# Performance work log

Measured on AMD Instinct MI355X. Metric: run time of the kernel, lower is better.

Reference implementation:

```python
import jax, jax.numpy as jnp
import numpy as np

WS, OWS, HEADS, DIM = 16, 24, 6, 192
PAD = (OWS - WS) // 2
NQ, NKV = WS * WS, OWS * OWS
TABLE = (WS + OWS - 1) ** 2


def _rpi():
    # replicates WindowsHandling.get_relative_position_index_for_overlap_window
    c = np.arange(WS)
    ori = np.stack(np.meshgrid(c, c, indexing='ij')).reshape(2, -1)
    e = np.arange(OWS)
    ext = np.stack(np.meshgrid(e, e, indexing='ij')).reshape(2, -1)
    rc = (ext[:, None, :] - ori[:, :, None]).transpose(1, 2, 0).astype(np.int64)
    rc[..., 0] += WS - OWS + 1
    rc[..., 1] += WS - OWS + 1
    rc[..., 0] *= WS + OWS - 1
    # mod mimics torch's negative advanced-index wraparound into the table
    return (rc.sum(-1) % TABLE).astype(np.int32)  # (NQ, NKV)


def _extract_patches(xp, nh, nw):
    # torch.nn.Unfold(kernel=OWS, stride=WS) equivalent on NHWC input.
    # xp: (b, PH, PW, c) -> (b*nh*nw, OWS*OWS, c), row-major window order.
    b, PH, PW, c = xp.shape
    i = (np.arange(nh) * WS)[:, None] + np.arange(OWS)[None, :]
    j = (np.arange(nw) * WS)[:, None] + np.arange(OWS)[None, :]
    t = jnp.take(xp, jnp.asarray(i.reshape(-1)), axis=1).reshape(b, nh, OWS, PW, c)
    t = jnp.take(t, jnp.asarray(j.reshape(-1)), axis=3).reshape(b, nh, OWS, nw, OWS, c)
    return t.transpose(0, 1, 3, 2, 4, 5).reshape(b * nh * nw, OWS * OWS, c)


def _attn_mask(h, w):
    # shift_size == 0 branch of get_attention_mask_for_overlap_window:
    # kv positions falling into the zero padding get -100.
    vm = np.zeros((1, h + 2 * PAD, w + 2 * PAD, 1), np.float32)
    vm[:, PAD:-PAD, PAD:-PAD, :] = 1.0
    nh, nw = h // WS, w // WS
    kv = np.asarray(_extract_patches(jnp.asarray(vm), nh, nw)).reshape(nh * nw, NKV)
    m = np.where(kv[:, None, :] > 0, 0.0, -100.0).astype(np.float32)
    return np.broadcast_to(m, (nh * nw, NQ, NKV)).copy()


def setup_inputs():
    key = jax.random.key(0)
    ks = jax.random.split(key, 8)
    b, h, w = 2, 160, 160
    s = 0.02
    return {
        'x': jax.random.normal(ks[0], (b, h, w, DIM), jnp.float32),
        'rpi': jnp.asarray(_rpi()),
        'attn_mask': jnp.asarray(_attn_mask(h, w)),
        'q_w': jax.random.normal(ks[1], (DIM, DIM), jnp.float32) * s,
        'q_b': jnp.zeros((DIM,), jnp.float32),
        'kv_w': jax.random.normal(ks[2], (DIM, 2 * DIM), jnp.float32) * s,
        'kv_b': jnp.zeros((2 * DIM,), jnp.float32),
        'bias_table': jax.random.normal(ks[3], (TABLE, HEADS), jnp.float32) * s,
        'gating_w': jax.random.normal(ks[4], (DIM, DIM), jnp.float32) * s,
        'gating_b': jnp.ones((DIM,), jnp.float32),
        'proj_w': jax.random.normal(ks[5], (DIM, DIM), jnp.float32) * s,
        'proj_b': jnp.zeros((DIM,), jnp.float32),
    }


def reference(x, rpi, attn_mask, q_w, q_b, kv_w, kv_b, bias_table, gating_w, gating_b, proj_w, proj_b):
    b, h, w, c = x.shape
    d = c // HEADS
    scale = d ** -0.5
    nh, nw = h // WS, w // WS
    nwin = nh * nw
    # shift_size == 0 path: zero-pad for overlapping kv windows
    x_pad = jnp.pad(x, ((0, 0), (PAD, PAD), (PAD, PAD), (0, 0)))
    # q windows (non-overlapping window partition)
    xw = x.reshape(b, nh, WS, nw, WS, c).transpose(0, 1, 3, 2, 4, 5).reshape(b * nwin, NQ, c)
    # kv windows (overlapping, Unfold equivalent)
    xpw = _extract_patches(x_pad, nh, nw)  # (b*nwin, NKV, c)
    gates = xw @ gating_w + gating_b                       # (b*nwin, NQ, c)
    q = (xw @ q_w + q_b).reshape(-1, NQ, HEADS, d).transpose(0, 2, 1, 3) * scale
    kv = xpw @ kv_w + kv_b
    k = kv[..., :c].reshape(-1, NKV, HEADS, d).transpose(0, 2, 1, 3)
    v = kv[..., c:].reshape(-1, NKV, HEADS, d).transpose(0, 2, 1, 3)
    attn = jnp.einsum('bhqd,bhkd->bhqk', q, k)             # (b*nwin, H, NQ, NKV)
    bias = bias_table[rpi.reshape(-1)].reshape(NQ, NKV, HEADS).transpose(2, 0, 1)
    attn = attn + bias[None]
    attn = attn.reshape(b, nwin, HEADS, NQ, NKV) + attn_mask[None, :, None]
    attn = jax.nn.softmax(attn, axis=-1).reshape(b * nwin, HEADS, NQ, NKV)
    out = jnp.einsum('bhqk,bhkd->bhqd', attn, v).transpose(0, 2, 1, 3).reshape(-1, NQ, c)
    out = out * gates
    out = out.reshape(b, nh, nw, WS, WS, c).transpose(0, 1, 3, 2, 4, 5).reshape(b, h, w, c)
    return out @ proj_w + proj_b
```

## Files before the change

### kernel.cpp

```cpp
#include <hip/hip_runtime.h>
#include <hip/hip_bf16.h>
#include <stdint.h>

typedef __bf16 bf16x8  __attribute__((ext_vector_type(8)));
typedef __bf16 bf16x4  __attribute__((ext_vector_type(4)));
typedef __bf16 bf16x16 __attribute__((ext_vector_type(16)));
typedef float  f32x4   __attribute__((ext_vector_type(4)));
typedef float  f32x16  __attribute__((ext_vector_type(16)));
typedef uint32_t u32;

#define MFMA16(a, b, c) __builtin_amdgcn_mfma_f32_16x16x32_bf16((a), (b), (c), 0, 0, 0)
#define MFMA32(a, b, c) __builtin_amdgcn_mfma_f32_32x32x16_bf16((a), (b), (c), 0, 0, 0)

constexpr int CH = 160, CW = 160, CC = 192, CHEADS = 6, CD = 32;
constexpr int CNQ = 256, CNKV = 576, CPH = 168;
constexpr float LOG2E = 1.44269504088896340736f;
constexpr float QSCALE_L2E = 0.17677669529663687f * 1.44269504088896340736f;

__global__ __launch_bounds__(256)
void biash_k(const int* __restrict__ rpi, const float* __restrict__ tab,
             __bf16* __restrict__ bth)
{
    int idx = blockIdx.x * 256 + threadIdx.x;
    int lane = idx & 63;
    int rest = idx >> 6;
    int ktg = rest % 18; rest /= 18;
    int qtg = rest & 7;
    int head = rest >> 3;
    int l31 = lane & 31, hi = lane >> 5;
    int q = qtg * 32 + l31;

    bf16x16 o16;
#pragma unroll
    for (int g = 0; g < 4; ++g) {
        int4 ri = *(const int4*)(rpi + q * CNKV + ktg * 32 + 4 * hi + g * 8);
        o16[g * 4 + 0] = (__bf16)(tab[ri.x * CHEADS + head] * LOG2E);
        o16[g * 4 + 1] = (__bf16)(tab[ri.y * CHEADS + head] * LOG2E);
        o16[g * 4 + 2] = (__bf16)(tab[ri.z * CHEADS + head] * LOG2E);
        o16[g * 4 + 3] = (__bf16)(tab[ri.w * CHEADS + head] * LOG2E);
    }
    *(bf16x16*)(bth + (long)idx * 16) = o16;
}

__global__ __launch_bounds__(256)
void mask_k(u32* __restrict__ mt)
{
    int idx = blockIdx.x * 256 + threadIdx.x;
    if (idx >= 9 * 18 * 64) return;
    int lane = idx & 63;
    int rest = idx >> 6;
    int ktg = rest % 18;
    int cls = rest / 18;
    int cy = cls / 3, cx = cls % 3;
    int hi = lane >> 5;
    u32 m = 0;
#pragma unroll
    for (int r = 0; r < 16; ++r) {
        int kv = ktg * 32 + 4 * hi + (r & 3) + 8 * (r >> 2);
        int oy = kv / 24, ox = kv - oy * 24;
        bool vy = (cy == 0) ? (oy >= 4) : ((cy == 2) ? (oy < 20) : true);
        bool vx = (cx == 0) ? (ox >= 4) : ((cx == 2) ? (ox < 20) : true);
        if (vy && vx) m |= (1u << r);
    }
    mt[idx] = m;
}

__global__ __launch_bounds__(256)
void wtrans_k(const float* __restrict__ q_w, const float* __restrict__ g_w,
              const float* __restrict__ kv_w, const float* __restrict__ p_w,
              const float* __restrict__ q_b, const float* __restrict__ g_b,
              const float* __restrict__ kv_b, const float* __restrict__ p_b,
              __bf16* __restrict__ Wt, __bf16* __restrict__ Wp,
              float* __restrict__ b768, float* __restrict__ pb)
{
    int idx = blockIdx.x * 256 + threadIdx.x;
    if (idx < 147456) {
        int n = idx / 192, k = idx - n * 192;
        float v;
        if (n < 192)      v = q_w[k * 192 + n] * QSCALE_L2E;
        else if (n < 384) v = g_w[k * 192 + (n - 192)];
        else              v = kv_w[k * 384 + (n - 384)];
        Wt[idx] = (__bf16)v;
    } else if (idx < 184320) {
        int j = idx - 147456;
        int n = j / 192, k = j - n * 192;
        Wp[j] = (__bf16)p_w[k * 192 + n];
    } else if (idx < 185280) {
        int j = idx - 184320;
        if (j < 192)      b768[j] = q_b[j] * QSCALE_L2E;
        else if (j < 384) b768[j] = g_b[j - 192];
        else if (j < 768) b768[j] = kv_b[j - 384];
        else              pb[j - 768] = p_b[j - 768];
    }
}

__global__ __launch_bounds__(256)
void padfill_k(const float* __restrict__ kv_b, __bf16* __restrict__ KVb)
{
    int tid = blockIdx.x * 256 + threadIdx.x;
    int row = tid / 48, seg = tid - row * 48;
    int bb = row / 2624, rr = row - bb * 2624;
    int py, px;
    if (rr < 672)       { py = rr / 168;               px = rr % 168; }
    else if (rr < 1344) { int r2 = rr - 672; py = 164 + r2 / 168; px = r2 % 168; }
    else                { int rm = rr - 1344; py = 4 + rm / 8; int q = rm & 7;
                          px = (q < 4) ? q : 160 + q; }
    bf16x8 v;
#pragma unroll
    for (int j = 0; j < 8; ++j) v[j] = (__bf16)kv_b[seg * 8 + j];
    *(bf16x8*)(KVb + ((long)((bb * CPH + py) * CPH + px)) * 384 + seg * 8) = v;
}

__global__ __launch_bounds__(256)
void gemm_f_k(const float* __restrict__ x, const __bf16* __restrict__ Wt,
              const float* __restrict__ b768,
              __bf16* __restrict__ Qb, __bf16* __restrict__ Gb,
              __bf16* __restrict__ KVb)
{
    __shared__ __bf16 As[2][4096];
    __shared__ __bf16 Bs[2][4096];

    const int bid = blockIdx.x;
    const int v = (bid & 7) * 1200 + (bid >> 3);
    const int bm = v / 12, bn = v - bm * 12;

    const int t = threadIdx.x, lane = t & 63, wv = t >> 6;
    const int l15 = lane & 15, l4 = lane >> 4;
    const int row = t >> 2, gp = t & 3;
    const int swz = row & 7;
    const int d0 = row * 64 + ((2 * gp) ^ swz) * 8;
    const int d1 = row * 64 + ((2 * gp + 1) ^ swz) * 8;

    const float*  asrc = x  + (long)(bm * 64 + row) * 192 + gp * 16;
    const __bf16* bsrc = Wt + (long)(bn * 64 + row) * 192 + gp * 16;

    float4 fa0, fa1, fa2, fa3;
    bf16x8 wb0, wb1;
    auto ld = [&](int kt) {
        const float* a = asrc + kt * 64;
        fa0 = ((const float4*)a)[0]; fa1 = ((const float4*)a)[1];
        fa2 = ((const float4*)a)[2]; fa3 = ((const float4*)a)[3];
        wb0 = *(const bf16x8*)(bsrc + kt * 64);
        wb1 = *(const bf16x8*)(bsrc + kt * 64 + 8);
    };
    auto st = [&](int buf) {
        bf16x8 g0, g1;
        g0[0] = (__bf16)fa0.x; g0[1] = (__bf16)fa0.y; g0[2] = (__bf16)fa0.z; g0[3] = (__bf16)fa0.w;
        g0[4] = (__bf16)fa1.x; g0[5] = (__bf16)fa1.y; g0[6] = (__bf16)fa1.z; g0[7] = (__bf16)fa1.w;
        g1[0] = (__bf16)fa2.x; g1[1] = (__bf16)fa2.y; g1[2] = (__bf16)fa2.z; g1[3] = (__bf16)fa2.w;
        g1[4] = (__bf16)fa3.x; g1[5] = (__bf16)fa3.y; g1[6] = (__bf16)fa3.z; g1[7] = (__bf16)fa3.w;
        *(bf16x8*)&As[buf][d0] = g0;
        *(bf16x8*)&As[buf][d1] = g1;
        *(bf16x8*)&Bs[buf][d0] = wb0;
        *(bf16x8*)&Bs[buf][d1] = wb1;
    };

    const int qm = (wv >> 1) * 32, qn = (wv & 1) * 32;
    f32x4 acc[2][2];
#pragma unroll
    for (int i = 0; i < 2; ++i)
#pragma unroll
        for (int j = 0; j < 2; ++j) acc[i][j] = f32x4{0.f, 0.f, 0.f, 0.f};

    ld(0);
    for (int kt = 0; kt < 3; ++kt) {
        const int buf = kt & 1;
        st(buf);
        if (kt < 2) ld(kt + 1);
        __syncthreads();
#pragma unroll
        for (int s = 0; s < 2; ++s) {
            bf16x8 af[2], bfr[2];
#pragma unroll
            for (int mi = 0; mi < 2; ++mi)
                af[mi] = *(const bf16x8*)&As[buf][(qm + mi * 16 + l15) * 64 +
                                                 (((s * 4 + l4) ^ (l15 & 7)) * 8)];
#pragma unroll
            for (int ni = 0; ni < 2; ++ni)
                bfr[ni] = *(const bf16x8*)&Bs[buf][(qn + ni * 16 + l15) * 64 +
                                                   (((s * 4 + l4) ^ (l15 & 7)) * 8)];
#pragma unroll
            for (int mi = 0; mi < 2; ++mi)
#pragma unroll
                for (int ni = 0; ni < 2; ++ni)
                    acc[mi][ni] = MFMA16(af[mi], bfr[ni], acc[mi][ni]);
        }
        __syncthreads();
    }

#pragma unroll
    for (int mi = 0; mi < 2; ++mi) {
#pragma unroll
        for (int r = 0; r < 4; ++r) {
            int rowg = bm * 64 + qm + mi * 16 + l4 * 4 + r;
            int bb = rowg / 25600, rr = rowg - bb * 25600;
            int y = rr / 160, xx = rr - y * 160;
            int win = bb * 100 + (y >> 4) * 10 + (xx >> 4);
            long widx = ((long)win * 256 + (y & 15) * 16 + (xx & 15)) * 192;
            long kidx = ((long)((bb * CPH + y + 4) * CPH + (xx + 4))) * 384;
#pragma unroll
            for (int ni = 0; ni < 2; ++ni) {
                int cg = bn * 64 + qn + ni * 16 + l15;
                float val = acc[mi][ni][r] + b768[cg];
                if (cg < 192)       Qb[widx + cg] = (__bf16)val;
                else if (cg < 384)  Gb[widx + cg - 192] = (__bf16)val;
                else                KVb[kidx + cg - 384] = (__bf16)val;
            }
        }
    }
}

__global__ __launch_bounds__(256)
void gemm_p_k(const __bf16* __restrict__ Yb, const __bf16* __restrict__ Wp,
              const float* __restrict__ pb, float* __restrict__ of)
{
    __shared__ __bf16 As[2][4096];
    __shared__ __bf16 Bs[2][4096];

    const int bid = blockIdx.x;
    const int v = (bid & 7) * 300 + (bid >> 3);
    const int bm = v / 3, bn = v - bm * 3;

    const int t = threadIdx.x, lane = t & 63, wv = t >> 6;
    const int l15 = lane & 15, l4 = lane >> 4;
    const int row = t >> 2, gp = t & 3;
    const int swz = row & 7;
    const int d0 = row * 64 + ((2 * gp) ^ swz) * 8;
    const int d1 = row * 64 + ((2 * gp + 1) ^ swz) * 8;

    const __bf16* asrc = Yb + (long)(bm * 64 + row) * 192 + gp * 16;
    const __bf16* bsrc = Wp + (long)(bn * 64 + row) * 192 + gp * 16;

    bf16x8 a0, a1, wb0, wb1;
    auto ld = [&](int kt) {
        a0  = *(const bf16x8*)(asrc + kt * 64);
        a1  = *(const bf16x8*)(asrc + kt * 64 + 8);
        wb0 = *(const bf16x8*)(bsrc + kt * 64);
        wb1 = *(const bf16x8*)(bsrc + kt * 64 + 8);
    };
    auto st = [&](int buf) {
        *(bf16x8*)&As[buf][d0] = a0;
        *(bf16x8*)&As[buf][d1] = a1;
        *(bf16x8*)&Bs[buf][d0] = wb0;
        *(bf16x8*)&Bs[buf][d1] = wb1;
    };

    const int qm = (wv >> 1) * 32, qn = (wv & 1) * 32;
    f32x4 acc[2][2];
#pragma unroll
    for (int i = 0; i < 2; ++i)
#pragma unroll
        for (int j = 0; j < 2; ++j) acc[i][j] = f32x4{0.f, 0.f, 0.f, 0.f};

    ld(0);
    for (int kt = 0; kt < 3; ++kt) {
        const int buf = kt & 1;
        st(buf);
        if (kt < 2) ld(kt + 1);
        __syncthreads();
#pragma unroll
        for (int s = 0; s < 2; ++s) {
            bf16x8 af[2], bfr[2];
#pragma unroll
            for (int mi = 0; mi < 2; ++mi)
                af[mi] = *(const bf16x8*)&As[buf][(qm + mi * 16 + l15) * 64 +
                                                 (((s * 4 + l4) ^ (l15 & 7)) * 8)];
#pragma unroll
            for (int ni = 0; ni < 2; ++ni)
                bfr[ni] = *(const bf16x8*)&Bs[buf][(qn + ni * 16 + l15) * 64 +
                                                   (((s * 4 + l4) ^ (l15 & 7)) * 8)];
#pragma unroll
            for (int mi = 0; mi < 2; ++mi)
#pragma unroll
                for (int ni = 0; ni < 2; ++ni)
                    acc[mi][ni] = MFMA16(af[mi], bfr[ni], acc[mi][ni]);
        }
        __syncthreads();
    }

#pragma unroll
    for (int mi = 0; mi < 2; ++mi) {
#pragma unroll
        for (int r = 0; r < 4; ++r) {
            int rowg = bm * 64 + qm + mi * 16 + l4 * 4 + r;
            int win = rowg >> 8, q = rowg & 255;
            int bb = win / 100, wr = win % 100;
            int y = (wr / 10) * 16 + (q >> 4), xx = (wr % 10) * 16 + (q & 15);
            long oidx = ((long)((bb * CH + y) * CW + xx)) * 192;
#pragma unroll
            for (int ni = 0; ni < 2; ++ni) {
                int cg = bn * 64 + qn + ni * 16 + l15;
                of[oidx + cg] = acc[mi][ni][r] + pb[cg];
            }
        }
    }
}

__global__ __launch_bounds__(512, 4)
void attn7_k(const __bf16* __restrict__ Q, const __bf16* __restrict__ KV,
             const __bf16* __restrict__ G, const __bf16* __restrict__ BTh,
             const u32* __restrict__ MT, __bf16* __restrict__ Y)
{
    __shared__ __bf16 Ks[576][36];
    __shared__ __bf16 Vt[32][580];

    const int bid = blockIdx.x;
    const int xs = bid & 7, ii = bid >> 3;
    const int win = xs * 25 + ii / 6;
    const int head = ii % 6;

    const int bb = win / 100, wr = win % 100, wy = wr / 10, wx = wr % 10;
    const int cy = (wy == 0) ? 0 : ((wy == 9) ? 2 : 1);
    const int cx = (wx == 0) ? 0 : ((wx == 9) ? 2 : 1);
    const int cls = cy * 3 + cx;
    const int t = threadIdx.x, lane = t & 63, wv = t >> 6;
    const int l31 = lane & 31, hi = lane >> 5;

    {
        const int pos0 = t >> 3, seg = t & 7;
        int oy = pos0 / 24, ox = pos0 - oy * 24;
        const long rowbase = ((long)((bb * CPH + wy * 16) * CPH + wx * 16)) * 384
                             + head * CD;
        int pos = pos0;
#pragma unroll
        for (int r = 0; r < 9; ++r) {
            const __bf16* p = KV + rowbase + (long)(oy * CPH + ox) * 384;
            if (seg < 4) {
                bf16x8 k8 = *(const bf16x8*)(p + seg * 8);
                *(bf16x8*)&Ks[pos][seg * 8] = k8;
            } else {
                bf16x8 v8 = *(const bf16x8*)(p + 192 + (seg - 4) * 8);
#pragma unroll
                for (int j = 0; j < 8; ++j) Vt[(seg - 4) * 8 + j][pos] = v8[j];
            }
            pos += 64;
            oy += 2; ox += 16;
            if (ox >= 24) { ox -= 24; oy += 1; }
        }
    }

    bf16x8 qf0, qf1;
    {
        const __bf16* qb = Q + ((long)win * CNQ + wv * 32 + l31) * CC + head * CD;
        qf0 = *(const bf16x8*)(qb + hi * 8);
        qf1 = *(const bf16x8*)(qb + 16 + hi * 8);
    }
    const __bf16* btb = BTh + (long)((head * 8 + wv) * 18) * 1024 + (long)lane * 16;
    bf16x16 bA = *(const bf16x16*)btb;

    __syncthreads();

    f32x16 o = {};
    float srun = 0.f;

    const char* kbase = (const char*)&Ks[0][0] + l31 * 72 + hi * 16;
    const char* vbase = (const char*)&Vt[0][0] + l31 * 1160 + hi * 8;

    bf16x8 kc0 = *(const bf16x8*)(kbase);
    bf16x8 kc1 = *(const bf16x8*)(kbase + 32);

    for (int tt = 0; tt < 18; ++tt) {
        bf16x8 kn0, kn1;
        bf16x16 bB;
        if (tt < 17) {
            const char* kn = kbase + (tt + 1) * 2304;
            kn0 = *(const bf16x8*)(kn);
            kn1 = *(const bf16x8*)(kn + 32);
            bB  = *(const bf16x16*)(btb + (long)(tt + 1) * 1024);
        }

        const char* vp = vbase + tt * 64;
        bf16x4 v00 = *(const bf16x4*)(vp);
        bf16x4 v01 = *(const bf16x4*)(vp + 16);
        bf16x4 v10 = *(const bf16x4*)(vp + 32);
        bf16x4 v11 = *(const bf16x4*)(vp + 48);
        bf16x8 vf0, vf1;
#pragma unroll
        for (int j = 0; j < 4; ++j) {
            vf0[j] = v00[j]; vf0[4 + j] = v01[j];
            vf1[j] = v10[j]; vf1[4 + j] = v11[j];
        }

        f32x16 st;
#pragma unroll
        for (int r = 0; r < 16; ++r) st[r] = (float)bA[r];
        __builtin_amdgcn_s_setprio(1);
        st = MFMA32(kc0, qf0, st);
        st = MFMA32(kc1, qf1, st);
        __builtin_amdgcn_s_setprio(0);

        const bool needm = (cx != 1) || (cy == 0 && tt < 3) || (cy == 2 && tt >= 15);
        u32 m = 0xFFFFFFFFu;
        if (needm) m = MT[(cls * 18 + tt) * 64 + lane];

        float p[16];
#pragma unroll
        for (int r = 0; r < 16; ++r) p[r] = exp2f(st[r]);
        if (needm) {
#pragma unroll
            for (int r = 0; r < 16; ++r)
                p[r] = (m & (1u << r)) ? p[r] : 0.0f;
        }
        float s = 0.f;
#pragma unroll
        for (int r = 0; r < 16; ++r) s += p[r];
        srun += s;

        bf16x8 pa0, pa1;
#pragma unroll
        for (int j = 0; j < 8; ++j) {
            pa0[j] = (__bf16)p[j];
            pa1[j] = (__bf16)p[8 + j];
        }

        __builtin_amdgcn_s_setprio(1);
        o = MFMA32(vf0, pa0, o);
        o = MFMA32(vf1, pa1, o);
        __builtin_amdgcn_s_setprio(0);

        kc0 = kn0; kc1 = kn1; bA = bB;
    }

    srun += __shfl_xor(srun, 32);
    float rs = 1.0f / srun;
    long base = ((long)win * CNQ + wv * 32 + l31) * CC + head * CD;
    const __bf16* gp2 = G + base;
    __bf16* yp = Y + base;
#pragma unroll
    for (int g = 0; g < 4; ++g) {
        bf16x4 gv = *(const bf16x4*)(gp2 + g * 8 + 4 * hi);
        bf16x4 ov;
#pragma unroll
        for (int j = 0; j < 4; ++j)
            ov[j] = (__bf16)(o[g * 4 + j] * rs * (float)gv[j]);
        *(bf16x4*)(yp + g * 8 + 4 * hi) = ov;
    }
}

extern "C" void kernel_launch(void* const* d_in, const int* in_sizes, int n_in,
                              void* d_out, int out_size, void* d_ws, size_t ws_size,
                              hipStream_t stream)
{
    (void)in_sizes; (void)n_in; (void)out_size; (void)ws_size;
    const float* x    = (const float*)d_in[0];
    const int*   rpi  = (const int*)  d_in[1];
    const float* q_w  = (const float*)d_in[3];
    const float* q_b  = (const float*)d_in[4];
    const float* kv_w = (const float*)d_in[5];
    const float* kv_b = (const float*)d_in[6];
    const float* btab = (const float*)d_in[7];
    const float* g_w  = (const float*)d_in[8];
    const float* g_b  = (const float*)d_in[9];
    const float* p_w  = (const float*)d_in[10];
    const float* p_b  = (const float*)d_in[11];
    float* out = (float*)d_out;

    char* ws = (char*)d_ws;
    __bf16* Qb  = (__bf16*)(ws);
    __bf16* KVb = (__bf16*)(ws + 19660800);
    __bf16* Gb  = (__bf16*)(ws + 63012864);
    __bf16* Yb  = (__bf16*)(ws + 82673664);
    __bf16* BTh = (__bf16*)(ws + 102334464);
    u32*    MT  = (u32*)   (ws + 104103936);
    __bf16* Wt  = (__bf16*)(ws + 104145408);
    __bf16* Wp  = (__bf16*)(ws + 104440320);
    float*  b768= (float*) (ws + 104514048);
    float*  pb  = (float*) (ws + 104517120);

    biash_k<<<216, 256, 0, stream>>>(rpi, btab, BTh);
    mask_k<<<41, 256, 0, stream>>>(MT);
    wtrans_k<<<724, 256, 0, stream>>>(q_w, g_w, kv_w, p_w, q_b, g_b, kv_b, p_b,
                                      Wt, Wp, b768, pb);
    padfill_k<<<984, 256, 0, stream>>>(kv_b, KVb);
    gemm_f_k<<<9600, 256, 0, stream>>>(x, Wt, b768, Qb, Gb, KVb);
    attn7_k<<<1200, 512, 0, stream>>>(Qb, KVb, Gb, BTh, MT, Yb);
    gemm_p_k<<<2400, 256, 0, stream>>>(Yb, Wp, pb, out);
}
```

Measured before the change: 155.9 us.

## Split K/V buffers, store V channel-planar, read V fragments directly from global

The projection GEMM now writes K into its own padded NHWC buffer and V into per-(batch, head, channel) planar images. The attention kernel drops its LDS V transpose and loads V MFMA fragments straight from global memory with walking pointers. Freeing that LDS allows a higher occupancy bound (6 blocks instead of 4). The cost is scattered 2-byte V stores in the GEMM epilogue, plus uncoalesced, latency-exposed global V loads inside the attention loop.

```diff
diff --git a/kernel.cpp b/kernel.cpp
--- a/kernel.cpp
+++ b/kernel.cpp
@@ -14,6 +14,7 @@
 
 constexpr int CH = 160, CW = 160, CC = 192, CHEADS = 6, CD = 32;
 constexpr int CNQ = 256, CNKV = 576, CPH = 168;
+constexpr int CPL = CPH * CPH;
 constexpr float LOG2E = 1.44269504088896340736f;
 constexpr float QSCALE_L2E = 0.17677669529663687f * 1.44269504088896340736f;
 
@@ -95,10 +96,11 @@
 }
 
 __global__ __launch_bounds__(256)
-void padfill_k(const float* __restrict__ kv_b, __bf16* __restrict__ KVb)
+void padk_k(const float* __restrict__ kv_b, __bf16* __restrict__ Kb)
 {
     int tid = blockIdx.x * 256 + threadIdx.x;
-    int row = tid / 48, seg = tid - row * 48;
+    if (tid >= 125952) return;
+    int row = tid / 24, seg = tid - row * 24;
     int bb = row / 2624, rr = row - bb * 2624;
     int py, px;
     if (rr < 672)       { py = rr / 168;               px = rr % 168; }
@@ -108,14 +110,42 @@
     bf16x8 v;
 #pragma unroll
     for (int j = 0; j < 8; ++j) v[j] = (__bf16)kv_b[seg * 8 + j];
-    *(bf16x8*)(KVb + ((long)((bb * CPH + py) * CPH + px)) * 384 + seg * 8) = v;
+    *(bf16x8*)(Kb + ((long)((bb * CPH + py) * CPH + px)) * 192 + seg * 8) = v;
+}
+
+__global__ __launch_bounds__(256)
+void padv_k(const float* __restrict__ kv_b, __bf16* __restrict__ VTg)
+{
+    int tid = blockIdx.x * 256 + threadIdx.x;
+    if (tid >= 125952) return;
+    int plane = tid / 328, c8 = (tid - plane * 328) * 8;
+    int d = plane & 31, head = (plane >> 5) % 6;
+    __bf16 val = (__bf16)kv_b[192 + head * 32 + d];
+    __bf16* base = VTg + (long)plane * CPL;
+    if (c8 < 1344) {
+        int py, px;
+        if (c8 < 672) { py = c8 / 168; px = c8 % 168; }
+        else          { int r2 = c8 - 672; py = 164 + r2 / 168; px = r2 % 168; }
+        bf16x8 v;
+#pragma unroll
+        for (int j = 0; j < 8; ++j) v[j] = val;
+        *(bf16x8*)(base + (long)py * CPH + px) = v;
+    } else {
+        int cm = c8 - 1344;
+        int py = 4 + cm / 8;
+        bf16x4 v;
+#pragma unroll
+        for (int j = 0; j < 4; ++j) v[j] = val;
+        *(bf16x4*)(base + (long)py * CPH) = v;
+        *(bf16x4*)(base + (long)py * CPH + 164) = v;
+    }
 }
 
 __global__ __launch_bounds__(256)
 void gemm_f_k(const float* __restrict__ x, const __bf16* __restrict__ Wt,
               const float* __restrict__ b768,
               __bf16* __restrict__ Qb, __bf16* __restrict__ Gb,
-              __bf16* __restrict__ KVb)
+              __bf16* __restrict__ Kb, __bf16* __restrict__ VTg)
 {
     __shared__ __bf16 As[2][4096];
     __shared__ __bf16 Bs[2][4096];
@@ -197,14 +227,20 @@
             int y = rr / 160, xx = rr - y * 160;
             int win = bb * 100 + (y >> 4) * 10 + (xx >> 4);
             long widx = ((long)win * 256 + (y & 15) * 16 + (xx & 15)) * 192;
-            long kidx = ((long)((bb * CPH + y + 4) * CPH + (xx + 4))) * 384;
+            long kidx = ((long)((bb * CPH + y + 4) * CPH + (xx + 4))) * 192;
+            long vpos = (long)(y + 4) * CPH + (xx + 4);
 #pragma unroll
             for (int ni = 0; ni < 2; ++ni) {
                 int cg = bn * 64 + qn + ni * 16 + l15;
                 float val = acc[mi][ni][r] + b768[cg];
                 if (cg < 192)       Qb[widx + cg] = (__bf16)val;
                 else if (cg < 384)  Gb[widx + cg - 192] = (__bf16)val;
-                else                KVb[kidx + cg - 384] = (__bf16)val;
+                else if (cg < 576)  Kb[kidx + cg - 384] = (__bf16)val;
+                else {
+                    int vv = cg - 576;
+                    int plane = (bb * 6 + (vv >> 5)) * 32 + (vv & 31);
+                    VTg[(long)plane * CPL + vpos] = (__bf16)val;
+                }
             }
         }
     }
@@ -296,13 +332,13 @@
     }
 }
 
-__global__ __launch_bounds__(512, 4)
-void attn7_k(const __bf16* __restrict__ Q, const __bf16* __restrict__ KV,
-             const __bf16* __restrict__ G, const __bf16* __restrict__ BTh,
-             const u32* __restrict__ MT, __bf16* __restrict__ Y)
+__global__ __launch_bounds__(512, 6)
+void attn8_k(const __bf16* __restrict__ Q, const __bf16* __restrict__ Kb,
+             const __bf16* __restrict__ VTg, const __bf16* __restrict__ G,
+             const __bf16* __restrict__ BTh, const u32* __restrict__ MT,
+             __bf16* __restrict__ Y)
 {
     __shared__ __bf16 Ks[576][36];
-    __shared__ __bf16 Vt[32][580];
 
     const int bid = blockIdx.x;
     const int xs = bid & 7, ii = bid >> 3;
@@ -317,24 +353,19 @@
     const int l31 = lane & 31, hi = lane >> 5;
 
     {
-        const int pos0 = t >> 3, seg = t & 7;
-        int oy = pos0 / 24, ox = pos0 - oy * 24;
-        const long rowbase = ((long)((bb * CPH + wy * 16) * CPH + wx * 16)) * 384
-                             + head * CD;
+        const int pos0 = t >> 2, seg = t & 3;
+        int oy = pos0 / 24, ox = pos0 % 24;
+        const __bf16* kb = Kb + ((long)((bb * CPH + wy * 16) * CPH + wx * 16)) * 192
+                           + head * 32 + seg * 8;
         int pos = pos0;
 #pragma unroll
-        for (int r = 0; r < 9; ++r) {
-            const __bf16* p = KV + rowbase + (long)(oy * CPH + ox) * 384;
-            if (seg < 4) {
-                bf16x8 k8 = *(const bf16x8*)(p + seg * 8);
+        for (int r = 0; r < 5; ++r) {
+            if (pos < 576) {
+                bf16x8 k8 = *(const bf16x8*)(kb + (long)(oy * CPH + ox) * 192);
                 *(bf16x8*)&Ks[pos][seg * 8] = k8;
-            } else {
-                bf16x8 v8 = *(const bf16x8*)(p + 192 + (seg - 4) * 8);
-#pragma unroll
-                for (int j = 0; j < 8; ++j) Vt[(seg - 4) * 8 + j][pos] = v8[j];
             }
-            pos += 64;
-            oy += 2; ox += 16;
+            pos += 128;
+            oy += 5; ox += 8;
             if (ox >= 24) { ox -= 24; oy += 1; }
         }
     }
@@ -348,14 +379,27 @@
     const __bf16* btb = BTh + (long)((head * 8 + wv) * 18) * 1024 + (long)lane * 16;
     bf16x16 bA = *(const bf16x16*)btb;
 
+    const __bf16* vbase = VTg + ((long)((bb * 6 + head) * 32 + l31)) * CPL
+                          + (long)(wy * 16) * CPH + wx * 16;
+    const __bf16 *vp0, *vp1, *vp2, *vp3;
+    int ox0, ox1, ox2, ox3;
+    {
+        int k0 = 4 * hi,      k1 = 8 + 4 * hi;
+        int k2 = 16 + 4 * hi, k3 = 24 + 4 * hi;
+        ox0 = k0; ox1 = k1; ox2 = k2;
+        int oy3 = k3 / 24;  ox3 = k3 - oy3 * 24;
+        vp0 = vbase + ox0;
+        vp1 = vbase + ox1;
+        vp2 = vbase + ox2;
+        vp3 = vbase + oy3 * CPH + ox3;
+    }
+
     __syncthreads();
 
     f32x16 o = {};
     float srun = 0.f;
 
     const char* kbase = (const char*)&Ks[0][0] + l31 * 72 + hi * 16;
-    const char* vbase = (const char*)&Vt[0][0] + l31 * 1160 + hi * 8;
-
     bf16x8 kc0 = *(const bf16x8*)(kbase);
     bf16x8 kc1 = *(const bf16x8*)(kbase + 32);
 
@@ -369,24 +413,29 @@
             bB  = *(const bf16x16*)(btb + (long)(tt + 1) * 1024);
         }
 
-        const char* vp = vbase + tt * 64;
-        bf16x4 v00 = *(const bf16x4*)(vp);
-        bf16x4 v01 = *(const bf16x4*)(vp + 16);
-        bf16x4 v10 = *(const bf16x4*)(vp + 32);
-        bf16x4 v11 = *(const bf16x4*)(vp + 48);
+        bf16x4 v0 = *(const bf16x4*)vp0;
+        bf16x4 v1 = *(const bf16x4*)vp1;
+        bf16x4 v2 = *(const bf16x4*)vp2;
+        bf16x4 v3 = *(const bf16x4*)vp3;
+        {
+            bool w0 = ox0 >= 16; vp0 += w0 ? (2 * CPH - 16) : (CPH + 8); ox0 = w0 ? ox0 - 16 : ox0 + 8;
+            bool w1 = ox1 >= 16; vp1 += w1 ? (2 * CPH - 16) : (CPH + 8); ox1 = w1 ? ox1 - 16 : ox1 + 8;
+            bool w2 = ox2 >= 16; vp2 += w2 ? (2 * CPH - 16) : (CPH + 8); ox2 = w2 ? ox2 - 16 : ox2 + 8;
+            bool w3 = ox3 >= 16; vp3 += w3 ? (2 * CPH - 16) : (CPH + 8); ox3 = w3 ? ox3 - 16 : ox3 + 8;
+        }
         bf16x8 vf0, vf1;
 #pragma unroll
         for (int j = 0; j < 4; ++j) {
-            vf0[j] = v00[j]; vf0[4 + j] = v01[j];
-            vf1[j] = v10[j]; vf1[4 + j] = v11[j];
-        }
-
-        f32x16 st;
-#pragma unroll
-        for (int r = 0; r < 16; ++r) st[r] = (float)bA[r];
+            vf0[j] = v0[j]; vf0[4 + j] = v1[j];
+            vf1[j] = v2[j]; vf1[4 + j] = v3[j];
+        }
+
+        f32x16 stv;
+#pragma unroll
+        for (int r = 0; r < 16; ++r) stv[r] = (float)bA[r];
         __builtin_amdgcn_s_setprio(1);
-        st = MFMA32(kc0, qf0, st);
-        st = MFMA32(kc1, qf1, st);
+        stv = MFMA32(kc0, qf0, stv);
+        stv = MFMA32(kc1, qf1, stv);
         __builtin_amdgcn_s_setprio(0);
 
         const bool needm = (cx != 1) || (cy == 0 && tt < 3) || (cy == 2 && tt >= 15);
@@ -395,7 +444,7 @@
 
         float p[16];
 #pragma unroll
-        for (int r = 0; r < 16; ++r) p[r] = exp2f(st[r]);
+        for (int r = 0; r < 16; ++r) p[r] = exp2f(stv[r]);
         if (needm) {
 #pragma unroll
             for (int r = 0; r < 16; ++r)
@@ -457,7 +506,8 @@
 
     char* ws = (char*)d_ws;
     __bf16* Qb  = (__bf16*)(ws);
-    __bf16* KVb = (__bf16*)(ws + 19660800);
+    __bf16* Kb  = (__bf16*)(ws + 19660800);
+    __bf16* VTg = (__bf16*)(ws + 41336832);
     __bf16* Gb  = (__bf16*)(ws + 63012864);
     __bf16* Yb  = (__bf16*)(ws + 82673664);
     __bf16* BTh = (__bf16*)(ws + 102334464);
@@ -471,8 +521,9 @@
     mask_k<<<41, 256, 0, stream>>>(MT);
     wtrans_k<<<724, 256, 0, stream>>>(q_w, g_w, kv_w, p_w, q_b, g_b, kv_b, p_b,
                                       Wt, Wp, b768, pb);
-    padfill_k<<<984, 256, 0, stream>>>(kv_b, KVb);
-    gemm_f_k<<<9600, 256, 0, stream>>>(x, Wt, b768, Qb, Gb, KVb);
-    attn7_k<<<1200, 512, 0, stream>>>(Qb, KVb, Gb, BTh, MT, Yb);
+    padk_k<<<492, 256, 0, stream>>>(kv_b, Kb);
+    padv_k<<<492, 256, 0, stream>>>(kv_b, VTg);
+    gemm_f_k<<<9600, 256, 0, stream>>>(x, Wt, b768, Qb, Gb, Kb, VTg);
+    attn8_k<<<1200, 512, 0, stream>>>(Qb, Kb, VTg, Gb, BTh, MT, Yb);
     gemm_p_k<<<2400, 256, 0, stream>>>(Yb, Wp, pb, out);
 }
```

Result: slower. 282.1 us (+81.0%).

## Fuse prep kernels, stage GEMM epilogue via LDS, keep bias table in fp32

Applied to the files above, without the earlier changes.

Merges the four small setup kernels (bias table, mask, weight transpose, pad fill) into one launch with block-range dispatch, which removes three kernel launches. The first GEMM epilogue now writes its tile to shared memory and then emits 16-byte vector stores per row, replacing scattered 2-byte stores. The attention kernel reads the relative-position bias as fp32 and uses it directly as the MFMA accumulator, which drops the per-tile bf16-to-float conversions but doubles the bias bytes read.

```diff
diff --git a/kernel.cpp b/kernel.cpp
--- a/kernel.cpp
+++ b/kernel.cpp
@@ -18,97 +18,93 @@
 constexpr float QSCALE_L2E = 0.17677669529663687f * 1.44269504088896340736f;
 
 __global__ __launch_bounds__(256)
-void biash_k(const int* __restrict__ rpi, const float* __restrict__ tab,
-             __bf16* __restrict__ bth)
+void prep_k(const int* __restrict__ rpi, const float* __restrict__ tab,
+            const float* __restrict__ q_w, const float* __restrict__ g_w,
+            const float* __restrict__ kv_w, const float* __restrict__ p_w,
+            const float* __restrict__ q_b, const float* __restrict__ g_b,
+            const float* __restrict__ kv_b, const float* __restrict__ p_b,
+            float* __restrict__ BTf, u32* __restrict__ mt,
+            __bf16* __restrict__ Wt, __bf16* __restrict__ Wp,
+            float* __restrict__ b768, float* __restrict__ pb,
+            __bf16* __restrict__ KVb)
 {
-    int idx = blockIdx.x * 256 + threadIdx.x;
-    int lane = idx & 63;
-    int rest = idx >> 6;
-    int ktg = rest % 18; rest /= 18;
-    int qtg = rest & 7;
-    int head = rest >> 3;
-    int l31 = lane & 31, hi = lane >> 5;
-    int q = qtg * 32 + l31;
-
-    bf16x16 o16;
-#pragma unroll
-    for (int g = 0; g < 4; ++g) {
-        int4 ri = *(const int4*)(rpi + q * CNKV + ktg * 32 + 4 * hi + g * 8);
-        o16[g * 4 + 0] = (__bf16)(tab[ri.x * CHEADS + head] * LOG2E);
-        o16[g * 4 + 1] = (__bf16)(tab[ri.y * CHEADS + head] * LOG2E);
-        o16[g * 4 + 2] = (__bf16)(tab[ri.z * CHEADS + head] * LOG2E);
-        o16[g * 4 + 3] = (__bf16)(tab[ri.w * CHEADS + head] * LOG2E);
-    }
-    *(bf16x16*)(bth + (long)idx * 16) = o16;
-}
-
-__global__ __launch_bounds__(256)
-void mask_k(u32* __restrict__ mt)
-{
-    int idx = blockIdx.x * 256 + threadIdx.x;
-    if (idx >= 9 * 18 * 64) return;
-    int lane = idx & 63;
-    int rest = idx >> 6;
-    int ktg = rest % 18;
-    int cls = rest / 18;
-    int cy = cls / 3, cx = cls % 3;
-    int hi = lane >> 5;
-    u32 m = 0;
-#pragma unroll
-    for (int r = 0; r < 16; ++r) {
-        int kv = ktg * 32 + 4 * hi + (r & 3) + 8 * (r >> 2);
-        int oy = kv / 24, ox = kv - oy * 24;
-        bool vy = (cy == 0) ? (oy >= 4) : ((cy == 2) ? (oy < 20) : true);
-        bool vx = (cx == 0) ? (ox >= 4) : ((cx == 2) ? (ox < 20) : true);
-        if (vy && vx) m |= (1u << r);
-    }
-    mt[idx] = m;
-}
-
-__global__ __launch_bounds__(256)
-void wtrans_k(const float* __restrict__ q_w, const float* __restrict__ g_w,
-              const float* __restrict__ kv_w, const float* __restrict__ p_w,
-              const float* __restrict__ q_b, const float* __restrict__ g_b,
-              const float* __restrict__ kv_b, const float* __restrict__ p_b,
-              __bf16* __restrict__ Wt, __bf16* __restrict__ Wp,
-              float* __restrict__ b768, float* __restrict__ pb)
-{
-    int idx = blockIdx.x * 256 + threadIdx.x;
-    if (idx < 147456) {
-        int n = idx / 192, k = idx - n * 192;
-        float v;
-        if (n < 192)      v = q_w[k * 192 + n] * QSCALE_L2E;
-        else if (n < 384) v = g_w[k * 192 + (n - 192)];
-        else              v = kv_w[k * 384 + (n - 384)];
-        Wt[idx] = (__bf16)v;
-    } else if (idx < 184320) {
-        int j = idx - 147456;
-        int n = j / 192, k = j - n * 192;
-        Wp[j] = (__bf16)p_w[k * 192 + n];
-    } else if (idx < 185280) {
-        int j = idx - 184320;
-        if (j < 192)      b768[j] = q_b[j] * QSCALE_L2E;
-        else if (j < 384) b768[j] = g_b[j - 192];
-        else if (j < 768) b768[j] = kv_b[j - 384];
-        else              pb[j - 768] = p_b[j - 768];
-    }
-}
-
-__global__ __launch_bounds__(256)
-void padfill_k(const float* __restrict__ kv_b, __bf16* __restrict__ KVb)
-{
-    int tid = blockIdx.x * 256 + threadIdx.x;
-    int row = tid / 48, seg = tid - row * 48;
-    int bb = row / 2624, rr = row - bb * 2624;
-    int py, px;
-    if (rr < 672)       { py = rr / 168;               px = rr % 168; }
-    else if (rr < 1344) { int r2 = rr - 672; py = 164 + r2 / 168; px = r2 % 168; }
-    else                { int rm = rr - 1344; py = 4 + rm / 8; int q = rm & 7;
-                          px = (q < 4) ? q : 160 + q; }
-    bf16x8 v;
-#pragma unroll
-    for (int j = 0; j < 8; ++j) v[j] = (__bf16)kv_b[seg * 8 + j];
-    *(bf16x8*)(KVb + ((long)((bb * CPH + py) * CPH + px)) * 384 + seg * 8) = v;
+    const int bidg = blockIdx.x;
+    if (bidg < 216) {
+        int idx = bidg * 256 + threadIdx.x;
+        int lane = idx & 63;
+        int rest = idx >> 6;
+        int ktg = rest % 18; rest /= 18;
+        int qtg = rest & 7;
+        int head = rest >> 3;
+        int l31 = lane & 31, hi = lane >> 5;
+        int q = qtg * 32 + l31;
+        float bv[16];
+#pragma unroll
+        for (int g = 0; g < 4; ++g) {
+            int4 ri = *(const int4*)(rpi + q * CNKV + ktg * 32 + 4 * hi + g * 8);
+            bv[g * 4 + 0] = tab[ri.x * CHEADS + head] * LOG2E;
+            bv[g * 4 + 1] = tab[ri.y * CHEADS + head] * LOG2E;
+            bv[g * 4 + 2] = tab[ri.z * CHEADS + head] * LOG2E;
+            bv[g * 4 + 3] = tab[ri.w * CHEADS + head] * LOG2E;
+        }
+        float* dst = BTf + (long)idx * 16;
+#pragma unroll
+        for (int g = 0; g < 4; ++g)
+            *(float4*)(dst + g * 4) = *(float4*)&bv[g * 4];
+    } else if (bidg < 257) {
+        int idx = (bidg - 216) * 256 + threadIdx.x;
+        if (idx >= 9 * 18 * 64) return;
+        int lane = idx & 63;
+        int rest = idx >> 6;
+        int ktg = rest % 18;
+        int cls = rest / 18;
+        int cy = cls / 3, cx = cls % 3;
+        int hi = lane >> 5;
+        u32 m = 0;
+#pragma unroll
+        for (int r = 0; r < 16; ++r) {
+            int kv = ktg * 32 + 4 * hi + (r & 3) + 8 * (r >> 2);
+            int oy = kv / 24, ox = kv - oy * 24;
+            bool vy = (cy == 0) ? (oy >= 4) : ((cy == 2) ? (oy < 20) : true);
+            bool vx = (cx == 0) ? (ox >= 4) : ((cx == 2) ? (ox < 20) : true);
+            if (vy && vx) m |= (1u << r);
+        }
+        mt[idx] = m;
+    } else if (bidg < 981) {
+        int idx = (bidg - 257) * 256 + threadIdx.x;
+        if (idx < 147456) {
+            int n = idx / 192, k = idx - n * 192;
+            float v;
+            if (n < 192)      v = q_w[k * 192 + n] * QSCALE_L2E;
+            else if (n < 384) v = g_w[k * 192 + (n - 192)];
+            else              v = kv_w[k * 384 + (n - 384)];
+            Wt[idx] = (__bf16)v;
+        } else if (idx < 184320) {
+            int j = idx - 147456;
+            int n = j / 192, k = j - n * 192;
+            Wp[j] = (__bf16)p_w[k * 192 + n];
+        } else if (idx < 185280) {
+            int j = idx - 184320;
+            if (j < 192)      b768[j] = q_b[j] * QSCALE_L2E;
+            else if (j < 384) b768[j] = g_b[j - 192];
+            else if (j < 768) b768[j] = kv_b[j - 384];
+            else              pb[j - 768] = p_b[j - 768];
+        }
+    } else {
+        int tid = (bidg - 981) * 256 + threadIdx.x;
+        if (tid >= 251904) return;
+        int row = tid / 48, seg = tid - row * 48;
+        int bb = row / 2624, rr = row - bb * 2624;
+        int py, px;
+        if (rr < 672)       { py = rr / 168;               px = rr % 168; }
+        else if (rr < 1344) { int r2 = rr - 672; py = 164 + r2 / 168; px = r2 % 168; }
+        else                { int rm = rr - 1344; py = 4 + rm / 8; int q = rm & 7;
+                              px = (q < 4) ? q : 160 + q; }
+        bf16x8 v;
+#pragma unroll
+        for (int j = 0; j < 8; ++j) v[j] = (__bf16)kv_b[seg * 8 + j];
+        *(bf16x8*)(KVb + ((long)((bb * CPH + py) * CPH + px)) * 384 + seg * 8) = v;
+    }
 }
 
 __global__ __launch_bounds__(256)
@@ -188,24 +184,38 @@
         __syncthreads();
     }
 
-#pragma unroll
-    for (int mi = 0; mi < 2; ++mi) {
-#pragma unroll
-        for (int r = 0; r < 4; ++r) {
-            int rowg = bm * 64 + qm + mi * 16 + l4 * 4 + r;
-            int bb = rowg / 25600, rr = rowg - bb * 25600;
-            int y = rr / 160, xx = rr - y * 160;
+    __bf16* epi = &As[0][0];
+    float bv0 = b768[bn * 64 + qn + l15];
+    float bv1 = b768[bn * 64 + qn + 16 + l15];
+#pragma unroll
+    for (int mi = 0; mi < 2; ++mi)
+#pragma unroll
+        for (int ni = 0; ni < 2; ++ni)
+#pragma unroll
+            for (int r = 0; r < 4; ++r) {
+                int rowl = qm + mi * 16 + l4 * 4 + r;
+                int coll = qn + ni * 16 + l15;
+                epi[rowl * 80 + coll] =
+                    (__bf16)(acc[mi][ni][r] + (ni ? bv1 : bv0));
+            }
+    __syncthreads();
+#pragma unroll
+    for (int k = 0; k < 2; ++k) {
+        int rid = t * 2 + k;
+        int rowl = rid >> 3, seg = rid & 7;
+        bf16x8 vv = *(const bf16x8*)&epi[rowl * 80 + seg * 8];
+        int rowg = bm * 64 + rowl;
+        int bb = rowg / 25600, rr = rowg - bb * 25600;
+        int y = rr / 160, xx = rr - y * 160;
+        int cg = bn * 64 + seg * 8;
+        if (bn < 6) {
             int win = bb * 100 + (y >> 4) * 10 + (xx >> 4);
             long widx = ((long)win * 256 + (y & 15) * 16 + (xx & 15)) * 192;
+            if (bn < 3) *(bf16x8*)(Qb + widx + cg) = vv;
+            else        *(bf16x8*)(Gb + widx + cg - 192) = vv;
+        } else {
             long kidx = ((long)((bb * CPH + y + 4) * CPH + (xx + 4))) * 384;
-#pragma unroll
-            for (int ni = 0; ni < 2; ++ni) {
-                int cg = bn * 64 + qn + ni * 16 + l15;
-                float val = acc[mi][ni][r] + b768[cg];
-                if (cg < 192)       Qb[widx + cg] = (__bf16)val;
-                else if (cg < 384)  Gb[widx + cg - 192] = (__bf16)val;
-                else                KVb[kidx + cg - 384] = (__bf16)val;
-            }
+            *(bf16x8*)(KVb + kidx + cg - 384) = vv;
         }
     }
 }
@@ -297,8 +307,8 @@
 }
 
 __global__ __launch_bounds__(512, 4)
-void attn7_k(const __bf16* __restrict__ Q, const __bf16* __restrict__ KV,
-             const __bf16* __restrict__ G, const __bf16* __restrict__ BTh,
+void attn9_k(const __bf16* __restrict__ Q, const __bf16* __restrict__ KV,
+             const __bf16* __restrict__ G, const float* __restrict__ BTf,
              const u32* __restrict__ MT, __bf16* __restrict__ Y)
 {
     __shared__ __bf16 Ks[576][36];
@@ -345,8 +355,8 @@
         qf0 = *(const bf16x8*)(qb + hi * 8);
         qf1 = *(const bf16x8*)(qb + 16 + hi * 8);
     }
-    const __bf16* btb = BTh + (long)((head * 8 + wv) * 18) * 1024 + (long)lane * 16;
-    bf16x16 bA = *(const bf16x16*)btb;
+    const float* btb = BTf + (long)((head * 8 + wv) * 18) * 1024 + (long)lane * 16;
+    f32x16 bA = *(const f32x16*)btb;
 
     __syncthreads();
 
@@ -361,32 +371,30 @@
 
     for (int tt = 0; tt < 18; ++tt) {
         bf16x8 kn0, kn1;
-        bf16x16 bB;
+        f32x16 bB;
         if (tt < 17) {
             const char* kn = kbase + (tt + 1) * 2304;
             kn0 = *(const bf16x8*)(kn);
             kn1 = *(const bf16x8*)(kn + 32);
-            bB  = *(const bf16x16*)(btb + (long)(tt + 1) * 1024);
+            bB  = *(const f32x16*)(btb + (long)(tt + 1) * 1024);
         }
 
         const char* vp = vbase + tt * 64;
-        bf16x4 v00 = *(const bf16x4*)(vp);
-        bf16x4 v01 = *(const bf16x4*)(vp + 16);
-        bf16x4 v10 = *(const bf16x4*)(vp + 32);
-        bf16x4 v11 = *(const bf16x4*)(vp + 48);
+        bf16x4 v0 = *(const bf16x4*)(vp);
+        bf16x4 v1 = *(const bf16x4*)(vp + 16);
+        bf16x4 v2 = *(const bf16x4*)(vp + 32);
+        bf16x4 v3 = *(const bf16x4*)(vp + 48);
         bf16x8 vf0, vf1;
 #pragma unroll
         for (int j = 0; j < 4; ++j) {
-            vf0[j] = v00[j]; vf0[4 + j] = v01[j];
-            vf1[j] = v10[j]; vf1[4 + j] = v11[j];
-        }
-
-        f32x16 st;
-#pragma unroll
-        for (int r = 0; r < 16; ++r) st[r] = (float)bA[r];
+            vf0[j] = v0[j]; vf0[4 + j] = v1[j];
+            vf1[j] = v2[j]; vf1[4 + j] = v3[j];
+        }
+
+        f32x16 stv = bA;
         __builtin_amdgcn_s_setprio(1);
-        st = MFMA32(kc0, qf0, st);
-        st = MFMA32(kc1, qf1, st);
+        stv = MFMA32(kc0, qf0, stv);
+        stv = MFMA32(kc1, qf1, stv);
         __builtin_amdgcn_s_setprio(0);
 
         const bool needm = (cx != 1) || (cy == 0 && tt < 3) || (cy == 2 && tt >= 15);
@@ -395,7 +403,7 @@
 
         float p[16];
 #pragma unroll
-        for (int r = 0; r < 16; ++r) p[r] = exp2f(st[r]);
+        for (int r = 0; r < 16; ++r) p[r] = exp2f(stv[r]);
         if (needm) {
 #pragma unroll
             for (int r = 0; r < 16; ++r)
@@ -460,19 +468,17 @@
     __bf16* KVb = (__bf16*)(ws + 19660800);
     __bf16* Gb  = (__bf16*)(ws + 63012864);
     __bf16* Yb  = (__bf16*)(ws + 82673664);
-    __bf16* BTh = (__bf16*)(ws + 102334464);
-    u32*    MT  = (u32*)   (ws + 104103936);
-    __bf16* Wt  = (__bf16*)(ws + 104145408);
-    __bf16* Wp  = (__bf16*)(ws + 104440320);
-    float*  b768= (float*) (ws + 104514048);
-    float*  pb  = (float*) (ws + 104517120);
-
-    biash_k<<<216, 256, 0, stream>>>(rpi, btab, BTh);
-    mask_k<<<41, 256, 0, stream>>>(MT);
-    wtrans_k<<<724, 256, 0, stream>>>(q_w, g_w, kv_w, p_w, q_b, g_b, kv_b, p_b,
-                                      Wt, Wp, b768, pb);
-    padfill_k<<<984, 256, 0, stream>>>(kv_b, KVb);
+    float*  BTf = (float*) (ws + 102334464);
+    u32*    MT  = (u32*)   (ws + 105873408);
+    __bf16* Wt  = (__bf16*)(ws + 105914880);
+    __bf16* Wp  = (__bf16*)(ws + 106209792);
+    float*  b768= (float*) (ws + 106283520);
+    float*  pb  = (float*) (ws + 106286592);
+
+    prep_k<<<1965, 256, 0, stream>>>(rpi, btab, q_w, g_w, kv_w, p_w,
+                                     q_b, g_b, kv_b, p_b,
+                                     BTf, MT, Wt, Wp, b768, pb, KVb);
     gemm_f_k<<<9600, 256, 0, stream>>>(x, Wt, b768, Qb, Gb, KVb);
-    attn7_k<<<1200, 512, 0, stream>>>(Qb, KVb, Gb, BTh, MT, Yb);
+    attn9_k<<<1200, 512, 0, stream>>>(Qb, KVb, Gb, BTf, MT, Yb);
     gemm_p_k<<<2400, 256, 0, stream>>>(Yb, Wp, pb, out);
 }
```

Measured after the change: 147.6 us. 5.3% less time.
